# Kernel tuning notes

Hardware: AMD Instinct MI355X
Metric: run time of the kernel (lower is better)

## Reference

```python
import jax, jax.numpy as jnp
import numpy as np

Q_DIM = 1024
K_DIM = 1024
EMBED_DIM = 1024
NUM_HEADS = 16
HEAD_DIM = EMBED_DIM // NUM_HEADS
SCALE = HEAD_DIM ** (-0.5)
CLAMP = 50000.0
MASK_NEG = -9e15


def _xavier(key, out_f, in_f):
    limit = float(np.sqrt(6.0 / (in_f + out_f)))
    return jax.random.uniform(key, (out_f, in_f), jnp.float32, -limit, limit)


def setup_inputs() -> dict:
    key = jax.random.key(0)
    ks = jax.random.split(key, 8)
    B, Tq, Tk = 4, 2048, 2048
    return {
        "q": jax.random.normal(ks[0], (B, Tq, Q_DIM), jnp.float32),
        "k": jax.random.normal(ks[1], (B, Tk, K_DIM), jnp.float32),
        "v": jax.random.normal(ks[2], (B, Tk, K_DIM), jnp.float32),
        "attention_mask": jax.random.randint(ks[3], (B, Tk), 0, 2, jnp.int32),
        "Wq": _xavier(ks[4], EMBED_DIM, Q_DIM),
        "bq": jnp.zeros((EMBED_DIM,), jnp.float32),
        "Wk": _xavier(ks[5], EMBED_DIM, K_DIM),
        "bk": jnp.zeros((EMBED_DIM,), jnp.float32),
        "Wv": _xavier(ks[6], EMBED_DIM, K_DIM),
        "bv": jnp.zeros((EMBED_DIM,), jnp.float32),
        "Wo": _xavier(ks[7], K_DIM, EMBED_DIM),
        "bo": jnp.zeros((K_DIM,), jnp.float32),
    }


def _split_heads(x, B, T):
    # [B, T, E] -> [B, H, T, D]
    return x.reshape(B, T, NUM_HEADS, HEAD_DIM).transpose(0, 2, 1, 3)


def reference(q, k, v, attention_mask, Wq, bq, Wk, bk, Wv, bv, Wo, bo):
    B, Tq, _ = q.shape
    Tk = k.shape[1]
    # projections (nn.Linear: x @ W.T + b)
    qs = _split_heads((q @ Wq.T + bq) * SCALE, B, Tq)   # [B,H,Tq,D]
    ks_ = _split_heads(k @ Wk.T + bk, B, Tk)            # [B,H,Tk,D]
    vs = _split_heads(v @ Wv.T + bv, B, Tk)             # [B,H,Tk,D]
    # scores with clamp
    scores = jnp.einsum("bhqd,bhkd->bhqk", qs, ks_)
    scores = jnp.clip(scores, -CLAMP, CLAMP)
    # additive mask: masked_fill(mask==0, -9e15) then add (nonzero entries add their value)
    m = attention_mask.astype(scores.dtype)
    add_mask = jnp.where(attention_mask == 0, MASK_NEG, m)  # [B,Tk]
    scores = scores + add_mask[:, None, None, :]
    probs = jax.nn.softmax(scores, axis=-1)
    # dropout inactive in eval mode
    attn = jnp.einsum("bhqk,bhkd->bhqd", probs, vs)
    attn = attn.transpose(0, 2, 1, 3).reshape(B, Tq, EMBED_DIM)
    return attn @ Wo.T + bo
```

## Files before the change

### kernel.cpp

```cpp
#include <hip/hip_runtime.h>
#include <hip/hip_bf16.h>

typedef __bf16 bf16x8 __attribute__((ext_vector_type(8)));
typedef float  f32x4  __attribute__((ext_vector_type(4)));
typedef unsigned short ushort;
typedef ushort ushort4v __attribute__((ext_vector_type(4)));

__device__ __forceinline__ ushort f2bf(float f) {
  union { float f; unsigned u; } v; v.f = f;
  unsigned r = v.u + 0x7FFFu + ((v.u >> 16) & 1u);
  return (ushort)(r >> 16);
}

typedef __attribute__((address_space(1))) const unsigned int as1_uint;
typedef __attribute__((address_space(3))) unsigned int as3_uint;
__device__ __forceinline__ void gll16(const void* g, void* l) {
  __builtin_amdgcn_global_load_lds((as1_uint*)g, (as3_uint*)l, 16, 0, 0);
}

__global__ void prep(const float* __restrict__ Wq, const float* __restrict__ Wk,
                     const float* __restrict__ Wv, const float* __restrict__ Wo,
                     const int* __restrict__ mask,
                     ushort4v* __restrict__ wqb, ushort4v* __restrict__ wkb,
                     ushort4v* __restrict__ wvb, ushort4v* __restrict__ wob,
                     float* __restrict__ madd) {
  int y = blockIdx.y;
  if (y == 4) {
    int i = blockIdx.x * blockDim.x + threadIdx.x;
    if (i < 8192) { int mv = mask[i]; madd[i] = (mv == 0) ? -9e15f : (float)mv; }
    return;
  }
  const float* s = (y == 0) ? Wq : (y == 1) ? Wk : (y == 2) ? Wv : Wo;
  ushort4v* d = (y == 0) ? wqb : (y == 1) ? wkb : (y == 2) ? wvb : wob;
  const float4* s4p = (const float4*)s;
  const int n4 = 1024 * 1024 / 4;
  for (int i = blockIdx.x * blockDim.x + threadIdx.x; i < n4; i += gridDim.x * blockDim.x) {
    float4 v = s4p[i]; ushort4v o;
    o[0] = f2bf(v.x); o[1] = f2bf(v.y); o[2] = f2bf(v.z); o[3] = f2bf(v.w);
    d[i] = o;
  }
}

__global__ void cast3(const float* __restrict__ q, const float* __restrict__ k,
                      const float* __restrict__ v,
                      ushort4v* __restrict__ qb, ushort4v* __restrict__ kb,
                      ushort4v* __restrict__ vb) {
  int y = blockIdx.y;
  const float4* s = (const float4*)((y == 0) ? q : (y == 1) ? k : v);
  ushort4v* d = (y == 0) ? qb : (y == 1) ? kb : vb;
  const int n4 = 8192 * 1024 / 4;
  for (int i = blockIdx.x * blockDim.x + threadIdx.x; i < n4; i += gridDim.x * blockDim.x) {
    float4 vv = s[i]; ushort4v o;
    o[0] = f2bf(vv.x); o[1] = f2bf(vv.y); o[2] = f2bf(vv.z); o[3] = f2bf(vv.w);
    d[i] = o;
  }
}

__device__ __forceinline__ void gemm_core(
    const ushort* __restrict__ A, const ushort* __restrict__ W,
    const float* __restrict__ bias, void* __restrict__ outp,
    float scale, int mode, ushort* smem)
{
  const int tid = threadIdx.x, lane = tid & 63, wid = tid >> 6;
  const int r0 = blockIdx.y * 128, c0 = blockIdx.x * 128;
  const int wr = (wid >> 1) * 64, wc = (wid & 1) * 64;
  const int K = 1024;
  ushort* sA = smem;
  ushort* sB = smem + 8192;

  f32x4 acc[4][4] = {};

  for (int kt = 0; kt < 16; ++kt) {
    const int k0 = kt * 64;
#pragma unroll
    for (int i = 0; i < 4; ++i) {
      int s = (wid * 4 + i) * 64 + lane;
      int row = s >> 3, sl = s & 7, gsl = sl ^ (row & 7);
      gll16(&A[(size_t)(r0 + row) * K + k0 + gsl * 8], &sA[(wid * 4 + i) * 512]);
      gll16(&W[(size_t)(c0 + row) * K + k0 + gsl * 8], &sB[(wid * 4 + i) * 512]);
    }
    __syncthreads();
#pragma unroll
    for (int kk = 0; kk < 2; ++kk) {
      bf16x8 af[4], bf[4];
#pragma unroll
      for (int mf = 0; mf < 4; ++mf) {
        int row = wr + mf * 16 + (lane & 15);
        int slot = (kk * 4 + (lane >> 4)) ^ (row & 7);
        af[mf] = *(const bf16x8*)&sA[row * 64 + slot * 8];
      }
#pragma unroll
      for (int nf = 0; nf < 4; ++nf) {
        int row = wc + nf * 16 + (lane & 15);
        int slot = (kk * 4 + (lane >> 4)) ^ (row & 7);
        bf[nf] = *(const bf16x8*)&sB[row * 64 + slot * 8];
      }
#pragma unroll
      for (int mf = 0; mf < 4; ++mf)
#pragma unroll
        for (int nf = 0; nf < 4; ++nf)
          acc[mf][nf] = __builtin_amdgcn_mfma_f32_16x16x32_bf16(af[mf], bf[nf], acc[mf][nf], 0, 0, 0);
    }
    __syncthreads();
  }

  if (mode == 2) {
    ushort* sT = smem;
#pragma unroll
    for (int nf = 0; nf < 4; ++nf) {
      int col = wc + nf * 16 + (lane & 15);
      float bv = bias[c0 + col];
#pragma unroll
      for (int mf = 0; mf < 4; ++mf)
#pragma unroll
        for (int r = 0; r < 4; ++r) {
          int row = wr + mf * 16 + ((lane >> 4) * 4) + r;
          sT[col * 128 + (row ^ ((col & 7) << 3))] = f2bf(acc[mf][nf][r] + bv);
        }
    }
    __syncthreads();
    int bidx = r0 >> 11, tb = r0 & 2047;
#pragma unroll
    for (int it = 0; it < 8; ++it) {
      int colr = it * 16 + wid * 4 + (lane >> 4);
      int t0 = (lane & 15) * 8;
      int4 v = *(const int4*)&sT[colr * 128 + (t0 ^ ((colr & 7) << 3))];
      int colg = c0 + colr;
      int hh = colg >> 6, d = colg & 63;
      *(int4*)&((ushort*)outp)[((size_t)(bidx * 16 + hh) * 64 + d) * 2048 + tb + t0] = v;
    }
    return;
  }

#pragma unroll
  for (int nf = 0; nf < 4; ++nf) {
    int col = c0 + wc + nf * 16 + (lane & 15);
    float bv = bias[col];
#pragma unroll
    for (int mf = 0; mf < 4; ++mf) {
#pragma unroll
      for (int r = 0; r < 4; ++r) {
        int row = r0 + wr + mf * 16 + ((lane >> 4) * 4) + r;
        float v = (acc[mf][nf][r] + bv) * scale;
        if (mode == 0) {
          int b = row >> 11, t = row & 2047;
          int h = col >> 6, d = col & 63;
          ((ushort*)outp)[(((size_t)(b * 16 + h) * 2048 + t) << 6) + d] = f2bf(v);
        } else {
          ((float*)outp)[(size_t)row * 1024 + col] = v;
        }
      }
    }
  }
}

__global__ __launch_bounds__(256) void gemm3(
    const ushort* __restrict__ qb, const ushort* __restrict__ kb, const ushort* __restrict__ vb,
    const ushort* __restrict__ wq, const ushort* __restrict__ wk, const ushort* __restrict__ wv,
    const float* __restrict__ bq, const float* __restrict__ bk, const float* __restrict__ bv,
    ushort* __restrict__ Qs, ushort* __restrict__ Ks, ushort* __restrict__ Vts)
{
  __shared__ __align__(16) ushort smem[16384];
  int z = blockIdx.z;
  const ushort *A, *W; const float* bias; ushort* out; float scale; int mode;
  if (z == 0)      { A = qb; W = wq; bias = bq; out = Qs;  scale = 0.125f; mode = 0; }
  else if (z == 1) { A = kb; W = wk; bias = bk; out = Ks;  scale = 1.0f;   mode = 0; }
  else             { A = vb; W = wv; bias = bv; out = Vts; scale = 1.0f;   mode = 2; }
  gemm_core(A, W, bias, out, scale, mode, smem);
}

__global__ __launch_bounds__(256) void gemmF(
    const ushort* __restrict__ Oat, const ushort* __restrict__ wo,
    const float* __restrict__ bo, float* __restrict__ out)
{
  __shared__ __align__(16) ushort smem[16384];
  gemm_core(Oat, wo, bo, out, 1.0f, 1, smem);
}

__global__ __launch_bounds__(256) void attn(
    const ushort* __restrict__ Q, const ushort* __restrict__ Km,
    const ushort* __restrict__ Vt, const float* __restrict__ madd,
    ushort* __restrict__ O)
{
  __shared__ __align__(16) ushort sQ[64 * 64];
  __shared__ __align__(16) ushort sK[64 * 64];
  __shared__ __align__(16) ushort sVt[64 * 64];
  __shared__ __align__(16) ushort sP[4 * 16 * 64];

  const int tid = threadIdx.x, lane = tid & 63, wid = tid >> 6;
  const int bid = blockIdx.x;
  const int x = bid & 7, g = bid >> 3;
  const int pair = x * 8 + (g >> 5), qt = g & 31;
  const int b = pair >> 4, h = pair & 15;

  const size_t hb = (size_t)pair * (2048 * 64);
  const ushort* Qh = Q + hb + (size_t)qt * (64 * 64);
  const ushort* Kh = Km + hb;
  const ushort* Vh = Vt + hb;
  const float* mb = madd + b * 2048;

  const int m = lane & 15, qg = lane >> 4;

#pragma unroll
  for (int c = 0; c < 2; ++c) {
    int s = tid + c * 256, row = s >> 3, sl = s & 7, ssl = sl ^ (row & 7);
    *(int4*)&sQ[row * 64 + ssl * 8] = *(const int4*)&Qh[row * 64 + sl * 8];
  }

  const int sr0 = tid >> 3,         sl0 = tid & 7,         ssl0 = sl0 ^ (sr0 & 7);
  const int sr1 = (tid + 256) >> 3, sl1 = (tid + 256) & 7, ssl1 = sl1 ^ (sr1 & 7);

  int4 kreg0 = *(const int4*)&Kh[(size_t)sr0 * 64 + sl0 * 8];
  int4 kreg1 = *(const int4*)&Kh[(size_t)sr1 * 64 + sl1 * 8];
  int4 vreg0 = *(const int4*)&Vh[(size_t)sr0 * 2048 + sl0 * 8];
  int4 vreg1 = *(const int4*)&Vh[(size_t)sr1 * 2048 + sl1 * 8];

  __syncthreads();
  bf16x8 qf[2];
#pragma unroll
  for (int kk = 0; kk < 2; ++kk) {
    int qrow = wid * 16 + m;
    int slot = (kk * 4 + qg) ^ (qrow & 7);
    qf[kk] = *(const bf16x8*)&sQ[qrow * 64 + slot * 8];
  }

  float runm = -3.0e38f, runl = 0.f;
  f32x4 o[4] = {};

  for (int kt = 0; kt < 32; ++kt) {
    if (kt) __syncthreads();
    *(int4*)&sK[sr0 * 64 + ssl0 * 8] = kreg0;
    *(int4*)&sK[sr1 * 64 + ssl1 * 8] = kreg1;
    *(int4*)&sVt[sr0 * 64 + ssl0 * 8] = vreg0;
    *(int4*)&sVt[sr1 * 64 + ssl1 * 8] = vreg1;
    __syncthreads();
    if (kt < 31) {
      const int n0n = (kt + 1) * 64;
      kreg0 = *(const int4*)&Kh[(size_t)(n0n + sr0) * 64 + sl0 * 8];
      kreg1 = *(const int4*)&Kh[(size_t)(n0n + sr1) * 64 + sl1 * 8];
      vreg0 = *(const int4*)&Vh[(size_t)sr0 * 2048 + n0n + sl0 * 8];
      vreg1 = *(const int4*)&Vh[(size_t)sr1 * 2048 + n0n + sl1 * 8];
    }
    const int n0 = kt * 64;
    float4 msk[4];
#pragma unroll
    for (int af = 0; af < 4; ++af)
      msk[af] = *(const float4*)&mb[n0 + af * 16 + qg * 4];

    f32x4 s4[4] = {};
    __builtin_amdgcn_s_setprio(1);
#pragma unroll
    for (int af = 0; af < 4; ++af) {
#pragma unroll
      for (int kk = 0; kk < 2; ++kk) {
        int krow = af * 16 + m;
        int slot = (kk * 4 + qg) ^ (krow & 7);
        bf16x8 kf = *(const bf16x8*)&sK[krow * 64 + slot * 8];
        s4[af] = __builtin_amdgcn_mfma_f32_16x16x32_bf16(kf, qf[kk], s4[af], 0, 0, 0);
      }
    }
    __builtin_amdgcn_s_setprio(0);

    float tmax = -3.0e38f;
#pragma unroll
    for (int af = 0; af < 4; ++af) {
      const float* mp = (const float*)&msk[af];
#pragma unroll
      for (int r = 0; r < 4; ++r) {
        float sv = fminf(fmaxf(s4[af][r], -50000.f), 50000.f) + mp[r];
        s4[af][r] = sv;
        tmax = fmaxf(tmax, sv);
      }
    }
    tmax = fmaxf(tmax, __shfl_xor(tmax, 16, 64));
    tmax = fmaxf(tmax, __shfl_xor(tmax, 32, 64));
    if (!__all(tmax <= runm + 8.f)) {
      float newm = fmaxf(runm, tmax);
      float corr = __expf(runm - newm);
      runl *= corr;
#pragma unroll
      for (int af = 0; af < 4; ++af) o[af] *= corr;
      runm = newm;
    }
    float psum = 0.f;
#pragma unroll
    for (int af = 0; af < 4; ++af) {
#pragma unroll
      for (int r = 0; r < 4; ++r) {
        float p = __expf(s4[af][r] - runm);
        s4[af][r] = p;
        psum += p;
      }
    }
    psum += __shfl_xor(psum, 16, 64);
    psum += __shfl_xor(psum, 32, 64);
    runl += psum;

#pragma unroll
    for (int af = 0; af < 4; ++af) {
      ushort4v pk;
#pragma unroll
      for (int r = 0; r < 4; ++r) pk[r] = f2bf(s4[af][r]);
      int ncol = af * 16 + qg * 4;
      int slot = (ncol >> 3) ^ (m & 7);
      *(ushort4v*)&sP[wid * 1024 + m * 64 + slot * 8 + (ncol & 7)] = pk;
    }

    __builtin_amdgcn_s_setprio(1);
#pragma unroll
    for (int kk = 0; kk < 2; ++kk) {
      int slotp = (kk * 4 + qg) ^ (m & 7);
      bf16x8 pf = *(const bf16x8*)&sP[wid * 1024 + m * 64 + slotp * 8];
#pragma unroll
      for (int af = 0; af < 4; ++af) {
        int drow = af * 16 + m;
        int slot = (kk * 4 + qg) ^ (drow & 7);
        bf16x8 vf = *(const bf16x8*)&sVt[drow * 64 + slot * 8];
        o[af] = __builtin_amdgcn_mfma_f32_16x16x32_bf16(vf, pf, o[af], 0, 0, 0);
      }
    }
    __builtin_amdgcn_s_setprio(0);
  }

  float inv = 1.0f / runl;
  int tq = qt * 64 + wid * 16 + m;
  size_t obase = (((size_t)(b * 2048 + tq)) * 16 + h) * 64;
#pragma unroll
  for (int af = 0; af < 4; ++af) {
    ushort4v pk;
#pragma unroll
    for (int r = 0; r < 4; ++r) pk[r] = f2bf(o[af][r] * inv);
    *(ushort4v*)&O[obase + af * 16 + qg * 4] = pk;
  }
}

extern "C" void kernel_launch(void* const* d_in, const int* in_sizes, int n_in,
                              void* d_out, int out_size, void* d_ws, size_t ws_size,
                              hipStream_t stream) {
  const float* q  = (const float*)d_in[0];
  const float* k  = (const float*)d_in[1];
  const float* v  = (const float*)d_in[2];
  const int* mask = (const int*)d_in[3];
  const float* Wq = (const float*)d_in[4];
  const float* bq = (const float*)d_in[5];
  const float* Wk = (const float*)d_in[6];
  const float* bk = (const float*)d_in[7];
  const float* Wv = (const float*)d_in[8];
  const float* bv = (const float*)d_in[9];
  const float* Wo = (const float*)d_in[10];
  const float* bo = (const float*)d_in[11];
  float* out = (float*)d_out;

  const size_t NEED = (size_t)104 << 20;
  if (ws_size < NEED) return;

  char* ws = (char*)d_ws;
  ushort* WQb = (ushort*)(ws + ((size_t)0 << 20));
  ushort* WKb = (ushort*)(ws + ((size_t)2 << 20));
  ushort* WVb = (ushort*)(ws + ((size_t)4 << 20));
  ushort* WOb = (ushort*)(ws + ((size_t)6 << 20));
  ushort* qb  = (ushort*)(ws + ((size_t)8 << 20));
  ushort* kb  = (ushort*)(ws + ((size_t)24 << 20));
  ushort* vb  = (ushort*)(ws + ((size_t)40 << 20));
  ushort* Qs  = (ushort*)(ws + ((size_t)56 << 20));
  ushort* Ks  = (ushort*)(ws + ((size_t)72 << 20));
  ushort* Vts = (ushort*)(ws + ((size_t)88 << 20));
  ushort* Oat = qb;
  float* madd = (float*)d_out;

  prep<<<dim3(256, 5), dim3(256), 0, stream>>>(Wq, Wk, Wv, Wo, mask,
      (ushort4v*)WQb, (ushort4v*)WKb, (ushort4v*)WVb, (ushort4v*)WOb, madd);
  cast3<<<dim3(1024, 3), dim3(256), 0, stream>>>(q, k, v,
      (ushort4v*)qb, (ushort4v*)kb, (ushort4v*)vb);

  gemm3<<<dim3(8, 64, 3), dim3(256), 0, stream>>>(qb, kb, vb, WQb, WKb, WVb,
      bq, bk, bv, Qs, Ks, Vts);

  attn<<<dim3(2048), dim3(256), 0, stream>>>(Qs, Ks, Vts, madd, Oat);

  gemmF<<<dim3(8, 64), dim3(256), 0, stream>>>(Oat, WOb, bo, out);
}
```

Before: 285.3 us.

## Keep softmax probabilities in registers via permlane swaps and use exp2 domain

Folds log2(e) into the Q projection scale and the additive mask so softmax can use native exp2, and replaces the clamp with a med3-based clamp on rescaled bounds. The P tile no longer round-trips through LDS: probabilities are packed with v_cvt_pk_bf16_f32 and rearranged across lanes with permlane32/16 swaps to form the MFMA operand directly. Q fragments are loaded straight from global memory, and the per-batch mask row is staged once into LDS. This removes LDS traffic and the f2bf conversion code, but relies on gfx950-specific instructions and correct lane mapping.

```diff
diff --git a/kernel.cpp b/kernel.cpp
--- a/kernel.cpp
+++ b/kernel.cpp
@@ -5,6 +5,18 @@
 typedef float  f32x4  __attribute__((ext_vector_type(4)));
 typedef unsigned short ushort;
 typedef ushort ushort4v __attribute__((ext_vector_type(4)));
+
+#if __has_builtin(__builtin_amdgcn_exp2f)
+#define EXP2(x) __builtin_amdgcn_exp2f(x)
+#else
+#define EXP2(x) exp2f(x)
+#endif
+
+#if __has_builtin(__builtin_amdgcn_fmed3f)
+#define CLAMP2(x) __builtin_amdgcn_fmed3f((x), -72134.75f, 72134.75f)
+#else
+#define CLAMP2(x) fminf(fmaxf((x), -72134.75f), 72134.75f)
+#endif
 
 __device__ __forceinline__ ushort f2bf(float f) {
   union { float f; unsigned u; } v; v.f = f;
@@ -27,7 +39,10 @@
   int y = blockIdx.y;
   if (y == 4) {
     int i = blockIdx.x * blockDim.x + threadIdx.x;
-    if (i < 8192) { int mv = mask[i]; madd[i] = (mv == 0) ? -9e15f : (float)mv; }
+    if (i < 8192) {
+      int mv = mask[i];
+      madd[i] = (mv == 0) ? -9e15f * 1.44269504f : (float)mv * 1.44269504f;
+    }
     return;
   }
   const float* s = (y == 0) ? Wq : (y == 1) ? Wk : (y == 2) ? Wv : Wo;
@@ -163,7 +178,7 @@
   __shared__ __align__(16) ushort smem[16384];
   int z = blockIdx.z;
   const ushort *A, *W; const float* bias; ushort* out; float scale; int mode;
-  if (z == 0)      { A = qb; W = wq; bias = bq; out = Qs;  scale = 0.125f; mode = 0; }
+  if (z == 0)      { A = qb; W = wq; bias = bq; out = Qs;  scale = 0.125f * 1.44269504f; mode = 0; }
   else if (z == 1) { A = kb; W = wk; bias = bk; out = Ks;  scale = 1.0f;   mode = 0; }
   else             { A = vb; W = wv; bias = bv; out = Vts; scale = 1.0f;   mode = 2; }
   gemm_core(A, W, bias, out, scale, mode, smem);
@@ -182,10 +197,9 @@
     const ushort* __restrict__ Vt, const float* __restrict__ madd,
     ushort* __restrict__ O)
 {
-  __shared__ __align__(16) ushort sQ[64 * 64];
   __shared__ __align__(16) ushort sK[64 * 64];
   __shared__ __align__(16) ushort sVt[64 * 64];
-  __shared__ __align__(16) ushort sP[4 * 16 * 64];
+  __shared__ __align__(16) float sM[2048];
 
   const int tid = threadIdx.x, lane = tid & 63, wid = tid >> 6;
   const int bid = blockIdx.x;
@@ -202,10 +216,13 @@
   const int m = lane & 15, qg = lane >> 4;
 
 #pragma unroll
-  for (int c = 0; c < 2; ++c) {
-    int s = tid + c * 256, row = s >> 3, sl = s & 7, ssl = sl ^ (row & 7);
-    *(int4*)&sQ[row * 64 + ssl * 8] = *(const int4*)&Qh[row * 64 + sl * 8];
-  }
+  for (int c = 0; c < 2; ++c)
+    *(float4*)&sM[(tid + c * 256) * 4] = *(const float4*)&mb[(tid + c * 256) * 4];
+
+  bf16x8 qf[2];
+#pragma unroll
+  for (int kk = 0; kk < 2; ++kk)
+    qf[kk] = *(const bf16x8*)&Qh[(size_t)(wid * 16 + m) * 64 + kk * 32 + qg * 8];
 
   const int sr0 = tid >> 3,         sl0 = tid & 7,         ssl0 = sl0 ^ (sr0 & 7);
   const int sr1 = (tid + 256) >> 3, sl1 = (tid + 256) & 7, ssl1 = sl1 ^ (sr1 & 7);
@@ -214,15 +231,6 @@
   int4 kreg1 = *(const int4*)&Kh[(size_t)sr1 * 64 + sl1 * 8];
   int4 vreg0 = *(const int4*)&Vh[(size_t)sr0 * 2048 + sl0 * 8];
   int4 vreg1 = *(const int4*)&Vh[(size_t)sr1 * 2048 + sl1 * 8];
-
-  __syncthreads();
-  bf16x8 qf[2];
-#pragma unroll
-  for (int kk = 0; kk < 2; ++kk) {
-    int qrow = wid * 16 + m;
-    int slot = (kk * 4 + qg) ^ (qrow & 7);
-    qf[kk] = *(const bf16x8*)&sQ[qrow * 64 + slot * 8];
-  }
 
   float runm = -3.0e38f, runl = 0.f;
   f32x4 o[4] = {};
@@ -242,10 +250,6 @@
       vreg1 = *(const int4*)&Vh[(size_t)sr1 * 2048 + n0n + sl1 * 8];
     }
     const int n0 = kt * 64;
-    float4 msk[4];
-#pragma unroll
-    for (int af = 0; af < 4; ++af)
-      msk[af] = *(const float4*)&mb[n0 + af * 16 + qg * 4];
 
     f32x4 s4[4] = {};
     __builtin_amdgcn_s_setprio(1);
@@ -264,53 +268,56 @@
     float tmax = -3.0e38f;
 #pragma unroll
     for (int af = 0; af < 4; ++af) {
-      const float* mp = (const float*)&msk[af];
-#pragma unroll
-      for (int r = 0; r < 4; ++r) {
-        float sv = fminf(fmaxf(s4[af][r], -50000.f), 50000.f) + mp[r];
-        s4[af][r] = sv;
-        tmax = fmaxf(tmax, sv);
-      }
+      float4 mk = *(const float4*)&sM[n0 + af * 16 + qg * 4];
+      const float* mp = (const float*)&mk;
+#pragma unroll
+      for (int r = 0; r < 4; ++r)
+        s4[af][r] = CLAMP2(s4[af][r]) + mp[r];
+      tmax = fmaxf(tmax, fmaxf(fmaxf(s4[af][0], s4[af][1]),
+                               fmaxf(s4[af][2], s4[af][3])));
     }
     tmax = fmaxf(tmax, __shfl_xor(tmax, 16, 64));
     tmax = fmaxf(tmax, __shfl_xor(tmax, 32, 64));
-    if (!__all(tmax <= runm + 8.f)) {
+    if (!__all(tmax <= runm + 11.5416f)) {
       float newm = fmaxf(runm, tmax);
-      float corr = __expf(runm - newm);
+      float corr = EXP2(runm - newm);
       runl *= corr;
 #pragma unroll
       for (int af = 0; af < 4; ++af) o[af] *= corr;
       runm = newm;
     }
+
     float psum = 0.f;
+    unsigned w[4][2];
 #pragma unroll
     for (int af = 0; af < 4; ++af) {
 #pragma unroll
       for (int r = 0; r < 4; ++r) {
-        float p = __expf(s4[af][r] - runm);
+        float p = EXP2(s4[af][r] - runm);
         s4[af][r] = p;
         psum += p;
       }
+      asm("v_cvt_pk_bf16_f32 %0, %1, %2"
+          : "=v"(w[af][0]) : "v"(s4[af][0]), "v"(s4[af][1]));
+      asm("v_cvt_pk_bf16_f32 %0, %1, %2"
+          : "=v"(w[af][1]) : "v"(s4[af][2]), "v"(s4[af][3]));
     }
     psum += __shfl_xor(psum, 16, 64);
     psum += __shfl_xor(psum, 32, 64);
     runl += psum;
 
-#pragma unroll
-    for (int af = 0; af < 4; ++af) {
-      ushort4v pk;
-#pragma unroll
-      for (int r = 0; r < 4; ++r) pk[r] = f2bf(s4[af][r]);
-      int ncol = af * 16 + qg * 4;
-      int slot = (ncol >> 3) ^ (m & 7);
-      *(ushort4v*)&sP[wid * 1024 + m * 64 + slot * 8 + (ncol & 7)] = pk;
-    }
-
     __builtin_amdgcn_s_setprio(1);
 #pragma unroll
     for (int kk = 0; kk < 2; ++kk) {
-      int slotp = (kk * 4 + qg) ^ (m & 7);
-      bf16x8 pf = *(const bf16x8*)&sP[wid * 1024 + m * 64 + slotp * 8];
+      unsigned a0 = w[2 * kk][0], a1 = w[2 * kk][1];
+      unsigned b0 = w[2 * kk + 1][0], b1 = w[2 * kk + 1][1];
+      asm("v_permlane32_swap_b32 %0, %1" : "+v"(a0), "+v"(b0));
+      asm("v_permlane16_swap_b32 %0, %1" : "+v"(a0), "+v"(b0));
+      asm("v_permlane32_swap_b32 %0, %1" : "+v"(a1), "+v"(b1));
+      asm("v_permlane16_swap_b32 %0, %1" : "+v"(a1), "+v"(b1));
+      union { unsigned u[4]; bf16x8 v; } pu;
+      pu.u[0] = a0; pu.u[1] = a1; pu.u[2] = b0; pu.u[3] = b1;
+      bf16x8 pf = pu.v;
 #pragma unroll
       for (int af = 0; af < 4; ++af) {
         int drow = af * 16 + m;
```

Result: faster. 258.0 us (-9.6%).
